# Kernel optimization log

Measured on AMD Instinct MI355X. Metric: run time of the kernel, lower is better.

The kernel has to match this reference:

```python
import jax, jax.numpy as jnp
import numpy as np

INPUT_DIM = 80
ENC_DIM = 256
ATTN_DIM = 128
GRU_DIM = 256
B = 32
T_ENC = 800
T_DEC = 400


def setup_inputs() -> dict:
    key = jax.random.key(0)
    ks = jax.random.split(key, 12)
    s = 0.05
    d = {}
    d['enc_feat'] = jax.random.normal(ks[0], (B, T_ENC, ENC_DIM), jnp.float32)
    d['ground_truth'] = jax.random.normal(ks[1], (B, T_DEC, INPUT_DIM), jnp.float32)
    # GRU (PyTorch layout): weight_ih (3*G, in), weight_hh (3*G, G)
    d['W_ih'] = jax.random.normal(ks[2], (3 * GRU_DIM, INPUT_DIM + ENC_DIM), jnp.float32) * s
    d['W_hh'] = jax.random.normal(ks[3], (3 * GRU_DIM, GRU_DIM), jnp.float32) * s
    d['b_ih'] = jax.random.normal(ks[4], (3 * GRU_DIM,), jnp.float32) * s
    d['b_hh'] = jax.random.normal(ks[5], (3 * GRU_DIM,), jnp.float32) * s
    # Additive attention: v^T tanh(W_enc e + W_dec h + b)
    d['W_enc'] = jax.random.normal(ks[6], (ATTN_DIM, ENC_DIM), jnp.float32) * s
    d['W_dec'] = jax.random.normal(ks[7], (ATTN_DIM, GRU_DIM), jnp.float32) * s
    d['b_attn'] = jax.random.normal(ks[8], (ATTN_DIM,), jnp.float32) * s
    d['v_attn'] = jax.random.normal(ks[9], (ATTN_DIM,), jnp.float32) * s
    # output_trans: Linear(gru_dim + enc_feat_dim -> input_dim)
    d['W_out'] = jax.random.normal(ks[10], (INPUT_DIM, GRU_DIM + ENC_DIM), jnp.float32) * s
    d['b_out'] = jax.random.normal(ks[11], (INPUT_DIM,), jnp.float32) * s
    return d


def reference(enc_feat, ground_truth, W_ih, W_hh, b_ih, b_hh,
              W_enc, W_dec, b_attn, v_attn, W_out, b_out):
    # Teacher-forced decode (teacher_force_rate=1.0): max_step = T_dec,
    # input at each step is ground_truth[:, t, :].
    Bsz, T_enc, E = enc_feat.shape
    G = W_hh.shape[1]
    # Encoder projection for additive attention (step-invariant)
    enc_proj = jnp.einsum('bte,ae->bta', enc_feat, W_enc)  # (B, T_enc, attn_dim)

    def step(carry, x_t):
        h, ctx = carry  # h: (B,G), ctx: (B,E)
        inp = jnp.concatenate([x_t, ctx], axis=-1)  # (B, input_dim+E)
        gi = inp @ W_ih.T + b_ih
        gh = h @ W_hh.T + b_hh
        ir, iz, inn = jnp.split(gi, 3, axis=-1)
        hr, hz, hn = jnp.split(gh, 3, axis=-1)
        r = jax.nn.sigmoid(ir + hr)
        z = jax.nn.sigmoid(iz + hz)
        n = jnp.tanh(inn + r * hn)
        h_new = (1.0 - z) * n + z * h  # PyTorch GRU update
        # additive attention over encoder timesteps
        dec_proj = h_new @ W_dec.T + b_attn  # (B, attn_dim)
        scores = jnp.einsum('bta,a->bt', jnp.tanh(enc_proj + dec_proj[:, None, :]), v_attn)
        attn = jax.nn.softmax(scores, axis=-1)  # (B, T_enc)
        ctx_new = jnp.einsum('bt,bte->be', attn, enc_feat)  # (B, E)
        concat = jnp.concatenate([h_new, ctx_new], axis=-1)
        pred = jax.nn.log_softmax(concat @ W_out.T + b_out, axis=-1)
        return (h_new, ctx_new), (pred, attn)

    h0 = jnp.zeros((Bsz, G), enc_feat.dtype)
    c0 = jnp.zeros((Bsz, E), enc_feat.dtype)
    xs = jnp.swapaxes(ground_truth, 0, 1)  # (T_dec, B, input_dim)
    _, (preds, attns) = jax.lax.scan(step, (h0, c0), xs)
    pred_seq = jnp.swapaxes(preds, 0, 1)    # (B, T_dec, input_dim)
    attn_record = jnp.swapaxes(attns, 0, 1)  # (B, T_dec, T_enc)
    return pred_seq, attn_record
```

## Files before the change

### kernel.cpp

```cpp
#include <hip/hip_runtime.h>

#define BB    32
#define TDEC  400
#define TENC  800
#define EDIM  256
#define GDIM  256
#define ADIM  128
#define IDIM  80
#define G3    768
#define NSL   16
#define SLH   16
#define SLT   50
#define FSTR  16
#define EPST  136
#define ETST  58

typedef unsigned short u16;
typedef unsigned int u32;

__device__ __forceinline__ float b2f(u16 u) {
  union { u32 i; float f; } x; x.i = ((u32)u) << 16; return x.f;
}
__device__ __forceinline__ u16 f2b(float f) {
  union { float f; u32 u; } x; x.f = f;
  u32 u = x.u; u += 0x7fffu + ((u >> 16) & 1u);
  return (u16)(u >> 16);
}
__device__ __forceinline__ void ld8(const u16* p, float* w) {
  const uint4 q = *reinterpret_cast<const uint4*>(p);
  union { u32 i; float f; } c;
  c.i = q.x << 16;          w[0] = c.f;
  c.i = q.x & 0xffff0000u;  w[1] = c.f;
  c.i = q.y << 16;          w[2] = c.f;
  c.i = q.y & 0xffff0000u;  w[3] = c.f;
  c.i = q.z << 16;          w[4] = c.f;
  c.i = q.z & 0xffff0000u;  w[5] = c.f;
  c.i = q.w << 16;          w[6] = c.f;
  c.i = q.w & 0xffff0000u;  w[7] = c.f;
}
__device__ __forceinline__ void ldf8(const float* p, float* w) {
  const float4 a = *reinterpret_cast<const float4*>(p);
  const float4 b = *reinterpret_cast<const float4*>(p + 4);
  w[0] = a.x; w[1] = a.y; w[2] = a.z; w[3] = a.w;
  w[4] = b.x; w[5] = b.y; w[6] = b.z; w[7] = b.w;
}
__device__ __forceinline__ float fsigmoid(float x) {
  return __builtin_amdgcn_rcpf(1.f + __expf(-x));
}
__device__ __forceinline__ float ftanh(float x) {
  float e = __expf(2.f * x);
  return 1.f - 2.f * __builtin_amdgcn_rcpf(e + 1.f);
}
__device__ __forceinline__ void ast(float* p, float v) {
  __hip_atomic_store(p, v, __ATOMIC_RELAXED, __HIP_MEMORY_SCOPE_AGENT);
}
__device__ __forceinline__ float ald(const float* p) {
  return __hip_atomic_load(p, __ATOMIC_RELAXED, __HIP_MEMORY_SCOPE_AGENT);
}
__device__ __forceinline__ void aadd(float* p, float v) {
  (void)__hip_atomic_fetch_add(p, v, __ATOMIC_RELAXED, __HIP_MEMORY_SCOPE_AGENT);
}

__global__ __launch_bounds__(256) void k_gix(
    const float* __restrict__ gt, const float* __restrict__ W_ih,
    const float* __restrict__ b_ih, u16* __restrict__ gi_x) {
  __shared__ float sc_x[8][IDIM];
  const int tid = threadIdx.x;
  const int b = blockIdx.x / 50;
  const int t0 = (blockIdx.x % 50) * 8;
  for (int idx = tid; idx < 8 * IDIM; idx += 256) {
    int row = idx / IDIM, col = idx % IDIM;
    sc_x[row][col] = gt[((size_t)b * TDEC + t0 + row) * IDIM + col];
  }
  __syncthreads();
  for (int kk = 0; kk < 3; ++kk) {
    const int g = tid + 256 * kk;
    const float* wrow = W_ih + (size_t)g * 336;
    float acc[8] = {0,0,0,0,0,0,0,0};
    #pragma unroll 2
    for (int k8 = 0; k8 < IDIM / 8; ++k8) {
      float w[8]; ldf8(wrow + (k8 << 3), w);
      #pragma unroll
      for (int tt = 0; tt < 8; ++tt) {
        const float* x = &sc_x[tt][k8 << 3];
        acc[tt] += w[0]*x[0] + w[1]*x[1] + w[2]*x[2] + w[3]*x[3]
                 + w[4]*x[4] + w[5]*x[5] + w[6]*x[6] + w[7]*x[7];
      }
    }
    const float bias = b_ih[g];
    #pragma unroll
    for (int tt = 0; tt < 8; ++tt)
      gi_x[((size_t)b * TDEC + t0 + tt) * G3 + g] = f2b(acc[tt] + bias);
  }
}

__global__ __launch_bounds__(256) void k_encp(
    const float* __restrict__ enc_feat, const float* __restrict__ W_enc,
    u16* __restrict__ encp, u16* __restrict__ enc_bf) {
  __shared__ float sc_x[16][EDIM];
  const int tid = threadIdx.x;
  const int b = blockIdx.x / 50;
  const int te0 = (blockIdx.x % 50) * 16;
  for (int idx = tid; idx < 16 * EDIM; idx += 256) {
    int row = idx >> 8, col = idx & 255;
    sc_x[row][col] = enc_feat[((size_t)b * TENC + te0 + row) * EDIM + col];
  }
  __syncthreads();
  const int a = tid & 127;
  const int tg = tid >> 7;
  const float* wrow = W_enc + (size_t)a * EDIM;
  float acc[8] = {0,0,0,0,0,0,0,0};
  #pragma unroll 4
  for (int k8 = 0; k8 < EDIM / 8; ++k8) {
    float w[8]; ldf8(wrow + (k8 << 3), w);
    #pragma unroll
    for (int tt = 0; tt < 8; ++tt) {
      const float* x = &sc_x[tg * 8 + tt][k8 << 3];
      acc[tt] += w[0]*x[0] + w[1]*x[1] + w[2]*x[2] + w[3]*x[3]
               + w[4]*x[4] + w[5]*x[5] + w[6]*x[6] + w[7]*x[7];
    }
  }
  #pragma unroll
  for (int tt = 0; tt < 8; ++tt)
    encp[((size_t)b * TENC + te0 + tg * 8 + tt) * ADIM + a] = f2b(acc[tt]);
  for (int idx = tid; idx < 16 * EDIM; idx += 256)
    enc_bf[((size_t)b * TENC + te0) * EDIM + idx] = f2b(sc_x[idx >> 8][idx & 255]);
}

__global__ __launch_bounds__(256, 2) void k_decode(
    const float* __restrict__ W_ih, const float* __restrict__ W_hh,
    const float* __restrict__ b_hh, const float* __restrict__ W_dec,
    const float* __restrict__ b_attn, const float* __restrict__ v_attn,
    const u16* __restrict__ gi_x, const u16* __restrict__ encp,
    const u16* __restrict__ enc_bf, float* __restrict__ stash,
    float* __restrict__ Xh, float* __restrict__ Dacc,
    float* __restrict__ Xctxacc, float* __restrict__ Xsumacc,
    int* __restrict__ flagA, int* __restrict__ flagB,
    float* __restrict__ out_attn) {
  __shared__ __align__(16) u16 encp_lds[SLT * EPST];
  __shared__ __align__(16) u16 enc_t[EDIM * ETST];
  __shared__ u32 sWdp[128 * 9];
  __shared__ __align__(16) float sc_h[256];
  __shared__ float sc_ing[4][68];
  __shared__ float sc_inh[4][68];
  __shared__ float sc_dec[ADIM];
  __shared__ float sc_g0[48];
  __shared__ float sc_g1[48];
  __shared__ float sc_w[56];
  __shared__ float sc_v[ADIM];
  __shared__ float sc_ba[ADIM];
  __shared__ float sc_bhh[48];
  __shared__ float sc_gx[48];
  __shared__ float sc_xs[4];

  const int tid = threadIdx.x;
  const int b = blockIdx.x & 31;
  const int j = blockIdx.x >> 5;
  const int lane = tid & 63;
  const int bank = j & 3;

  u32 wctx[32], whh[32];
  #pragma unroll
  for (int i = 0; i < 32; ++i) { wctx[i] = 0u; whh[i] = 0u; }
  if (tid < 192) {
    const int r = tid >> 2, q = tid & 3;
    const int grow = (r >> 4) * 256 + SLH * j + (r & 15);
    const float2* s1 = reinterpret_cast<const float2*>(
        W_ih + (size_t)grow * 336 + 80 + q * 64);
    const float2* s2 = reinterpret_cast<const float2*>(
        W_hh + (size_t)grow * 256 + q * 64);
    #pragma unroll
    for (int i = 0; i < 32; ++i) {
      const float2 v1 = s1[i], v2 = s2[i];
      wctx[i] = (u32)f2b(v1.x) | ((u32)f2b(v1.y) << 16);
      whh[i]  = (u32)f2b(v2.x) | ((u32)f2b(v2.y) << 16);
    }
  }
  for (int idx = tid; idx < 128 * 8; idx += 256) {
    const int a = idx >> 3, k2 = idx & 7;
    const float2 v = *reinterpret_cast<const float2*>(
        W_dec + (size_t)a * GDIM + SLH * j + 2 * k2);
    sWdp[a * 9 + k2] = (u32)f2b(v.x) | ((u32)f2b(v.y) << 16);
  }
  for (int idx = tid; idx < SLT * ADIM; idx += 256) {
    const int te = idx >> 7, a = idx & 127;
    encp_lds[te * EPST + a] = encp[((size_t)b * TENC + SLT * j + te) * ADIM + a];
  }
  for (int idx = tid; idx < SLT * EDIM; idx += 256) {
    const int te = idx >> 8, e = idx & 255;
    enc_t[e * ETST + te] = enc_bf[((size_t)b * TENC + SLT * j + te) * EDIM + e];
  }
  if (tid < ADIM) { sc_v[tid] = v_attn[tid]; sc_ba[tid] = b_attn[tid]; }
  if (tid < 48) {
    const int gate = tid >> 4, i = tid & 15;
    const int grow = gate * 256 + SLH * j + i;
    const float bh = b_hh[grow];
    sc_bhh[tid] = bh;
    sc_g1[tid] = bh;
    sc_gx[tid] = b2f(gi_x[((size_t)b * TDEC + 0) * G3 + grow]);
  }
  sc_h[tid] = 0.f;
  sc_ing[tid >> 6][tid & 63] = 0.f;
  sc_inh[tid >> 6][tid & 63] = 0.f;
  __syncthreads();

  for (int t = 0; t < TDEC; ++t) {
    const int p = t & 1;
    if (tid < 192) {
      const float* act = &sc_ing[tid & 3][0];
      float acc = 0.f;
      #pragma unroll
      for (int i = 0; i < 32; ++i) {
        union { u32 u; float f; } lo, hi;
        lo.u = wctx[i] << 16; hi.u = wctx[i] & 0xffff0000u;
        acc += lo.f * act[2 * i] + hi.f * act[2 * i + 1];
      }
      acc += __shfl_xor(acc, 1);
      acc += __shfl_xor(acc, 2);
      if ((tid & 3) == 0) sc_g0[tid >> 2] = acc + sc_gx[tid >> 2];
    }
    __syncthreads();
    if (tid < 64) {
      float hval = 0.f;
      if (lane < SLH) {
        const float gr = sc_g0[lane] + sc_g1[lane];
        const float gz = sc_g0[SLH + lane] + sc_g1[SLH + lane];
        const float rr = fsigmoid(gr);
        const float zz = fsigmoid(gz);
        const float nn = ftanh(sc_g0[2 * SLH + lane] + rr * sc_g1[2 * SLH + lane]);
        const float hp = sc_h[SLH * j + lane];
        hval = (1.f - zz) * nn + zz * hp;
        ast(&Xh[b * GDIM + SLH * j + lane], hval);
      }
      float hn16[16];
      #pragma unroll
      for (int k = 0; k < 16; ++k) hn16[k] = __shfl(hval, k);
      #pragma unroll
      for (int r2 = 0; r2 < 2; ++r2) {
        const int a = lane + 64 * r2;
        const u32* wp = &sWdp[a * 9];
        float acc = 0.f;
        #pragma unroll
        for (int k2 = 0; k2 < 8; ++k2) {
          const u32 w2 = wp[k2];
          union { u32 u; float f; } lo, hi;
          lo.u = w2 << 16; hi.u = w2 & 0xffff0000u;
          acc += lo.f * hn16[2 * k2] + hi.f * hn16[2 * k2 + 1];
        }
        aadd(&Dacc[((p * BB + b) * 4 + bank) * ADIM + a], acc);
      }
    }
    __syncthreads();
    if (tid == 0)
      __hip_atomic_store(&flagA[(b * NSL + j) * FSTR], t + 1, __ATOMIC_RELAXED,
                         __HIP_MEMORY_SCOPE_AGENT);
    if (tid < NSL) {
      const int* fp = &flagA[(b * NSL + tid) * FSTR];
      while (__hip_atomic_load(fp, __ATOMIC_RELAXED,
                               __HIP_MEMORY_SCOPE_AGENT) < t + 1)
        __builtin_amdgcn_s_sleep(1);
    }
    __syncthreads();
    {
      const float hv = ald(&Xh[b * GDIM + tid]);
      sc_h[tid] = hv;
      sc_inh[tid >> 6][tid & 63] = hv;
      if (j == 0) stash[((size_t)b * TDEC + t) * 512 + tid] = hv;
    }
    if (tid < ADIM) {
      float d = sc_ba[tid];
      #pragma unroll
      for (int k = 0; k < 4; ++k)
        d += ald(&Dacc[((p * BB + b) * 4 + k) * ADIM + tid]);
      sc_dec[tid] = d;
    }
    if (tid < 64) {
      const int w = j * 64 + tid;
      ast(&Xctxacc[(((1 - p) * BB + b) * 4 + (w >> 8)) * EDIM + (w & 255)], 0.f);
    } else if (tid < 96) {
      const int w = j * 32 + (tid - 64);
      ast(&Dacc[(((1 - p) * BB + b) * 4 + (w >> 7)) * ADIM + (w & 127)], 0.f);
    } else if (tid == 96 && j < 4) {
      ast(&Xsumacc[(((1 - p) * BB + b) * 4 + j) * FSTR], 0.f);
    }
    __syncthreads();
    if (tid < 200) {
      const int te = tid >> 2, q4 = tid & 3;
      const u16* ep = &encp_lds[te * EPST + q4 * 32];
      const float* dp = sc_dec + q4 * 32;
      const float* vp = sc_v + q4 * 32;
      float s = 0.f;
      #pragma unroll
      for (int k8 = 0; k8 < 4; ++k8) {
        float w[8]; ld8(ep + (k8 << 3), w);
        #pragma unroll
        for (int i = 0; i < 8; ++i) {
          const int a = (k8 << 3) + i;
          s += ftanh(w[i] + dp[a]) * vp[a];
        }
      }
      s += __shfl_xor(s, 1);
      s += __shfl_xor(s, 2);
      if (q4 == 0) sc_w[te] = __expf(s);
    } else if (tid < 248) {
      const int gl = tid - 200;
      const int grow = (gl >> 4) * 256 + SLH * j + (gl & 15);
      const int tn = (t + 1 < TDEC) ? t + 1 : t;
      sc_gx[gl] = b2f(gi_x[((size_t)b * TDEC + tn) * G3 + grow]);
    }
    __syncthreads();
    if (tid < 64) {
      float v = (tid < SLT) ? sc_w[tid] : 0.f;
      #pragma unroll
      for (int off = 1; off < 64; off <<= 1) v += __shfl_xor(v, off);
      if (tid == 0) aadd(&Xsumacc[((p * BB + b) * 4 + bank) * FSTR], v);
    }
    {
      const u32* et = reinterpret_cast<const u32*>(&enc_t[tid * ETST]);
      float pc = 0.f;
      #pragma unroll
      for (int k2 = 0; k2 < 25; ++k2) {
        const u32 w2 = et[k2];
        union { u32 u; float f; } lo, hi;
        lo.u = w2 << 16; hi.u = w2 & 0xffff0000u;
        pc += sc_w[2 * k2] * lo.f + sc_w[2 * k2 + 1] * hi.f;
      }
      aadd(&Xctxacc[((p * BB + b) * 4 + bank) * EDIM + tid], pc);
    }
    if (tid < 192) {
      const float* act = &sc_inh[tid & 3][0];
      float acc = 0.f;
      #pragma unroll
      for (int i = 0; i < 32; ++i) {
        union { u32 u; float f; } lo, hi;
        lo.u = whh[i] << 16; hi.u = whh[i] & 0xffff0000u;
        acc += lo.f * act[2 * i] + hi.f * act[2 * i + 1];
      }
      acc += __shfl_xor(acc, 1);
      acc += __shfl_xor(acc, 2);
      if ((tid & 3) == 0) sc_g1[tid >> 2] = acc + sc_bhh[tid >> 2];
    }
    __syncthreads();
    if (tid == 0)
      __hip_atomic_store(&flagB[(b * NSL + j) * FSTR], t + 1, __ATOMIC_RELAXED,
                         __HIP_MEMORY_SCOPE_AGENT);
    if (tid < NSL) {
      const int* fp = &flagB[(b * NSL + tid) * FSTR];
      while (__hip_atomic_load(fp, __ATOMIC_RELAXED,
                               __HIP_MEMORY_SCOPE_AGENT) < t + 1)
        __builtin_amdgcn_s_sleep(1);
      if (tid < 4) sc_xs[tid] = ald(&Xsumacc[((p * BB + b) * 4 + tid) * FSTR]);
    }
    __syncthreads();
    {
      const float S = sc_xs[0] + sc_xs[1] + sc_xs[2] + sc_xs[3];
      float c = 0.f;
      #pragma unroll
      for (int k = 0; k < 4; ++k)
        c += ald(&Xctxacc[((p * BB + b) * 4 + k) * EDIM + tid]);
      const float invS = __builtin_amdgcn_rcpf(S);
      const float cv = c * invS;
      sc_ing[tid >> 6][tid & 63] = cv;
      if (j == 0) stash[((size_t)b * TDEC + t) * 512 + 256 + tid] = cv;
      if (tid < SLT)
        out_attn[((size_t)b * TDEC + t) * TENC + SLT * j + tid] =
            sc_w[tid] * invS;
    }
    __syncthreads();
  }
}

__global__ __launch_bounds__(256) void k_pred(
    const float* __restrict__ stash, const float* __restrict__ W_out,
    const float* __restrict__ b_out, float* __restrict__ out_pred) {
  __shared__ float sc_s[4][512];
  __shared__ float sc_lp[2][4][IDIM];
  __shared__ float sc_l[4][IDIM];
  __shared__ float sc_lse[4];
  const int tid = threadIdx.x;
  const int b = blockIdx.x / 100;
  const int t0 = (blockIdx.x % 100) * 4;
  for (int idx = tid; idx < 4 * 512; idx += 256)
    sc_s[idx >> 9][idx & 511] = stash[((size_t)b * TDEC + t0) * 512 + idx];
  __syncthreads();
  const int o = tid & 127, kh = tid >> 7;
  if (o < IDIM) {
    const float* wrow = W_out + (size_t)o * 512 + kh * 256;
    float acc[4] = {0,0,0,0};
    #pragma unroll 4
    for (int k8 = 0; k8 < 32; ++k8) {
      float w[8]; ldf8(wrow + (k8 << 3), w);
      #pragma unroll
      for (int tt = 0; tt < 4; ++tt) {
        const float* x = &sc_s[tt][kh * 256 + (k8 << 3)];
        acc[tt] += w[0]*x[0] + w[1]*x[1] + w[2]*x[2] + w[3]*x[3]
                 + w[4]*x[4] + w[5]*x[5] + w[6]*x[6] + w[7]*x[7];
      }
    }
    #pragma unroll
    for (int tt = 0; tt < 4; ++tt) sc_lp[kh][tt][o] = acc[tt];
  }
  __syncthreads();
  if (tid < IDIM) {
    const float bb = b_out[tid];
    #pragma unroll
    for (int tt = 0; tt < 4; ++tt)
      sc_l[tt][tid] = sc_lp[0][tt][tid] + sc_lp[1][tt][tid] + bb;
  }
  __syncthreads();
  {
    const int w = tid >> 6, lane = tid & 63;
    const float a0 = sc_l[w][lane];
    const float a1 = (lane < IDIM - 64) ? sc_l[w][lane + 64] : -1e30f;
    float m = fmaxf(a0, a1);
    #pragma unroll
    for (int off = 1; off < 64; off <<= 1) m = fmaxf(m, __shfl_xor(m, off));
    float e = __expf(a0 - m) + ((lane < IDIM - 64) ? __expf(a1 - m) : 0.f);
    #pragma unroll
    for (int off = 1; off < 64; off <<= 1) e += __shfl_xor(e, off);
    if (lane == 0) sc_lse[w] = m + __logf(e);
  }
  __syncthreads();
  for (int idx = tid; idx < 4 * IDIM; idx += 256) {
    const int tt = idx / IDIM, oo = idx % IDIM;
    out_pred[((size_t)b * TDEC + t0 + tt) * IDIM + oo] =
        sc_l[tt][oo] - sc_lse[tt];
  }
}

extern "C" void kernel_launch(void* const* d_in, const int* in_sizes, int n_in,
                              void* d_out, int out_size, void* d_ws, size_t ws_size,
                              hipStream_t stream) {
  const float* enc_feat = (const float*)d_in[0];
  const float* gt       = (const float*)d_in[1];
  const float* W_ih     = (const float*)d_in[2];
  const float* W_hh     = (const float*)d_in[3];
  const float* b_ih     = (const float*)d_in[4];
  const float* b_hh     = (const float*)d_in[5];
  const float* W_enc    = (const float*)d_in[6];
  const float* W_dec    = (const float*)d_in[7];
  const float* b_attn   = (const float*)d_in[8];
  const float* v_attn   = (const float*)d_in[9];
  const float* W_out    = (const float*)d_in[10];
  const float* b_out    = (const float*)d_in[11];
  float* out_pred = (float*)d_out;
  float* out_attn = out_pred + (size_t)BB * TDEC * IDIM;

  char* ws = (char*)d_ws;
  size_t off = 0;
  u16* gi_x   = (u16*)(ws + off);   off += (size_t)BB * TDEC * G3 * 2;
  u16* encp   = (u16*)(ws + off);   off += (size_t)BB * TENC * ADIM * 2;
  u16* enc_bf = (u16*)(ws + off);   off += (size_t)BB * TENC * EDIM * 2;
  float* stash= (float*)(ws + off); off += (size_t)BB * TDEC * 512 * 4;
  float* Xh   = (float*)(ws + off); off += (size_t)BB * GDIM * 4;
  char* zbase = ws + off;
  int* flagA    = (int*)(ws + off);   off += (size_t)BB * NSL * FSTR * 4;
  int* flagB    = (int*)(ws + off);   off += (size_t)BB * NSL * FSTR * 4;
  float* Dacc   = (float*)(ws + off); off += (size_t)BB * 2 * 4 * ADIM * 4;
  float* Xctxacc= (float*)(ws + off); off += (size_t)BB * 2 * 4 * EDIM * 4;
  float* Xsumacc= (float*)(ws + off); off += (size_t)BB * 2 * 4 * FSTR * 4;
  const size_t zbytes = (size_t)(ws + off - zbase);

  hipMemsetAsync(zbase, 0, zbytes, stream);

  hipLaunchKernelGGL(k_gix, dim3(BB * 50), dim3(256), 0, stream,
                     gt, W_ih, b_ih, gi_x);
  hipLaunchKernelGGL(k_encp, dim3(BB * 50), dim3(256), 0, stream,
                     enc_feat, W_enc, encp, enc_bf);
  hipLaunchKernelGGL(k_decode, dim3(BB * NSL), dim3(256), 0, stream,
                     W_ih, W_hh, b_hh, W_dec, b_attn, v_attn,
                     gi_x, encp, enc_bf, stash, Xh, Dacc, Xctxacc, Xsumacc,
                     flagA, flagB, out_attn);
  hipLaunchKernelGGL(k_pred, dim3(BB * 100), dim3(256), 0, stream,
                     stash, W_out, b_out, out_pred);
}
```

Before: 3.388 ms.

## Halve decode slices per batch using 512-thread blocks with dynamic LDS

The persistent decode kernel now splits each batch row into 8 slices instead of 16. Each block runs 512 threads and owns 32 hidden units and 100 encoder timesteps. Encoder tiles move to dynamic shared memory, and per-slice arrays, the W_dec tile and thread-role ranges are resized to match. The aim is to cut the number of blocks taking part in each per-step cross-block flag barrier and the atomic partial-sum traffic. The cost is more per-block work and larger LDS use, and all 256 blocks must still be co-resident.

```diff
diff --git a/kernel.cpp b/kernel.cpp
--- a/kernel.cpp
+++ b/kernel.cpp
@@ -8,12 +8,12 @@
 #define ADIM  128
 #define IDIM  80
 #define G3    768
-#define NSL   16
-#define SLH   16
-#define SLT   50
+#define NSL   8
+#define SLH   32
+#define SLT   100
 #define FSTR  16
 #define EPST  136
-#define ETST  58
+#define ETST  102
 
 typedef unsigned short u16;
 typedef unsigned int u32;
@@ -127,7 +127,7 @@
     enc_bf[((size_t)b * TENC + te0) * EDIM + idx] = f2b(sc_x[idx >> 8][idx & 255]);
 }
 
-__global__ __launch_bounds__(256, 2) void k_decode(
+__global__ __launch_bounds__(512, 1) void k_decode(
     const float* __restrict__ W_ih, const float* __restrict__ W_hh,
     const float* __restrict__ b_hh, const float* __restrict__ W_dec,
     const float* __restrict__ b_attn, const float* __restrict__ v_attn,
@@ -137,20 +137,22 @@
     float* __restrict__ Xctxacc, float* __restrict__ Xsumacc,
     int* __restrict__ flagA, int* __restrict__ flagB,
     float* __restrict__ out_attn) {
-  __shared__ __align__(16) u16 encp_lds[SLT * EPST];
-  __shared__ __align__(16) u16 enc_t[EDIM * ETST];
-  __shared__ u32 sWdp[128 * 9];
+  extern __shared__ __align__(16) u16 dynlds[];
+  u16* encp_lds = dynlds;
+  u16* enc_t    = dynlds + SLT * EPST;
+
+  __shared__ u32 sWdp[ADIM * 17];
   __shared__ __align__(16) float sc_h[256];
   __shared__ float sc_ing[4][68];
   __shared__ float sc_inh[4][68];
   __shared__ float sc_dec[ADIM];
-  __shared__ float sc_g0[48];
-  __shared__ float sc_g1[48];
-  __shared__ float sc_w[56];
+  __shared__ float sc_g0[96];
+  __shared__ float sc_g1[96];
+  __shared__ float sc_w[104];
   __shared__ float sc_v[ADIM];
   __shared__ float sc_ba[ADIM];
-  __shared__ float sc_bhh[48];
-  __shared__ float sc_gx[48];
+  __shared__ float sc_bhh[96];
+  __shared__ float sc_gx[96];
   __shared__ float sc_xs[4];
 
   const int tid = threadIdx.x;
@@ -162,9 +164,9 @@
   u32 wctx[32], whh[32];
   #pragma unroll
   for (int i = 0; i < 32; ++i) { wctx[i] = 0u; whh[i] = 0u; }
-  if (tid < 192) {
+  if (tid < 384) {
     const int r = tid >> 2, q = tid & 3;
-    const int grow = (r >> 4) * 256 + SLH * j + (r & 15);
+    const int grow = (r >> 5) * 256 + SLH * j + (r & 31);
     const float2* s1 = reinterpret_cast<const float2*>(
         W_ih + (size_t)grow * 336 + 80 + q * 64);
     const float2* s2 = reinterpret_cast<const float2*>(
@@ -176,37 +178,38 @@
       whh[i]  = (u32)f2b(v2.x) | ((u32)f2b(v2.y) << 16);
     }
   }
-  for (int idx = tid; idx < 128 * 8; idx += 256) {
-    const int a = idx >> 3, k2 = idx & 7;
+  for (int idx = tid; idx < ADIM * 16; idx += 512) {
+    const int a = idx >> 4, k2 = idx & 15;
     const float2 v = *reinterpret_cast<const float2*>(
         W_dec + (size_t)a * GDIM + SLH * j + 2 * k2);
-    sWdp[a * 9 + k2] = (u32)f2b(v.x) | ((u32)f2b(v.y) << 16);
-  }
-  for (int idx = tid; idx < SLT * ADIM; idx += 256) {
+    sWdp[a * 17 + k2] = (u32)f2b(v.x) | ((u32)f2b(v.y) << 16);
+  }
+  for (int idx = tid; idx < SLT * ADIM; idx += 512) {
     const int te = idx >> 7, a = idx & 127;
     encp_lds[te * EPST + a] = encp[((size_t)b * TENC + SLT * j + te) * ADIM + a];
   }
-  for (int idx = tid; idx < SLT * EDIM; idx += 256) {
+  for (int idx = tid; idx < SLT * EDIM; idx += 512) {
     const int te = idx >> 8, e = idx & 255;
     enc_t[e * ETST + te] = enc_bf[((size_t)b * TENC + SLT * j + te) * EDIM + e];
   }
   if (tid < ADIM) { sc_v[tid] = v_attn[tid]; sc_ba[tid] = b_attn[tid]; }
-  if (tid < 48) {
-    const int gate = tid >> 4, i = tid & 15;
-    const int grow = gate * 256 + SLH * j + i;
+  if (tid < 96) {
+    const int grow = (tid >> 5) * 256 + SLH * j + (tid & 31);
     const float bh = b_hh[grow];
     sc_bhh[tid] = bh;
     sc_g1[tid] = bh;
     sc_gx[tid] = b2f(gi_x[((size_t)b * TDEC + 0) * G3 + grow]);
   }
-  sc_h[tid] = 0.f;
-  sc_ing[tid >> 6][tid & 63] = 0.f;
-  sc_inh[tid >> 6][tid & 63] = 0.f;
+  if (tid < 256) {
+    sc_h[tid] = 0.f;
+    sc_ing[tid >> 6][tid & 63] = 0.f;
+    sc_inh[tid >> 6][tid & 63] = 0.f;
+  }
   __syncthreads();
 
   for (int t = 0; t < TDEC; ++t) {
     const int p = t & 1;
-    if (tid < 192) {
+    if (tid < 384) {
       const float* act = &sc_ing[tid & 3][0];
       float acc = 0.f;
       #pragma unroll
@@ -232,20 +235,20 @@
         hval = (1.f - zz) * nn + zz * hp;
         ast(&Xh[b * GDIM + SLH * j + lane], hval);
       }
-      float hn16[16];
-      #pragma unroll
-      for (int k = 0; k < 16; ++k) hn16[k] = __shfl(hval, k);
+      float hn[32];
+      #pragma unroll
+      for (int k = 0; k < 32; ++k) hn[k] = __shfl(hval, k);
       #pragma unroll
       for (int r2 = 0; r2 < 2; ++r2) {
         const int a = lane + 64 * r2;
-        const u32* wp = &sWdp[a * 9];
+        const u32* wp = &sWdp[a * 17];
         float acc = 0.f;
         #pragma unroll
-        for (int k2 = 0; k2 < 8; ++k2) {
+        for (int k2 = 0; k2 < 16; ++k2) {
           const u32 w2 = wp[k2];
           union { u32 u; float f; } lo, hi;
           lo.u = w2 << 16; hi.u = w2 & 0xffff0000u;
-          acc += lo.f * hn16[2 * k2] + hi.f * hn16[2 * k2 + 1];
+          acc += lo.f * hn[2 * k2] + hi.f * hn[2 * k2 + 1];
         }
         aadd(&Dacc[((p * BB + b) * 4 + bank) * ADIM + a], acc);
       }
@@ -261,7 +264,7 @@
         __builtin_amdgcn_s_sleep(1);
     }
     __syncthreads();
-    {
+    if (tid < 256) {
       const float hv = ald(&Xh[b * GDIM + tid]);
       sc_h[tid] = hv;
       sc_inh[tid >> 6][tid & 63] = hv;
@@ -274,17 +277,17 @@
         d += ald(&Dacc[((p * BB + b) * 4 + k) * ADIM + tid]);
       sc_dec[tid] = d;
     }
-    if (tid < 64) {
-      const int w = j * 64 + tid;
+    if (tid >= 256 && tid < 384) {
+      const int w = j * 128 + (tid - 256);
       ast(&Xctxacc[(((1 - p) * BB + b) * 4 + (w >> 8)) * EDIM + (w & 255)], 0.f);
-    } else if (tid < 96) {
-      const int w = j * 32 + (tid - 64);
+    } else if (tid >= 384 && tid < 448) {
+      const int w = j * 64 + (tid - 384);
       ast(&Dacc[(((1 - p) * BB + b) * 4 + (w >> 7)) * ADIM + (w & 127)], 0.f);
-    } else if (tid == 96 && j < 4) {
+    } else if (tid == 448 && j < 4) {
       ast(&Xsumacc[(((1 - p) * BB + b) * 4 + j) * FSTR], 0.f);
     }
     __syncthreads();
-    if (tid < 200) {
+    if (tid < 400) {
       const int te = tid >> 2, q4 = tid & 3;
       const u16* ep = &encp_lds[te * EPST + q4 * 32];
       const float* dp = sc_dec + q4 * 32;
@@ -302,24 +305,31 @@
       s += __shfl_xor(s, 1);
       s += __shfl_xor(s, 2);
       if (q4 == 0) sc_w[te] = __expf(s);
-    } else if (tid < 248) {
-      const int gl = tid - 200;
-      const int grow = (gl >> 4) * 256 + SLH * j + (gl & 15);
+    } else if (tid >= 448) {
       const int tn = (t + 1 < TDEC) ? t + 1 : t;
-      sc_gx[gl] = b2f(gi_x[((size_t)b * TDEC + tn) * G3 + grow]);
+      const int gl = tid - 448;
+      {
+        const int grow = (gl >> 5) * 256 + SLH * j + (gl & 31);
+        sc_gx[gl] = b2f(gi_x[((size_t)b * TDEC + tn) * G3 + grow]);
+      }
+      if (gl < 32) {
+        const int g2 = gl + 64;
+        const int grow = (g2 >> 5) * 256 + SLH * j + (g2 & 31);
+        sc_gx[g2] = b2f(gi_x[((size_t)b * TDEC + tn) * G3 + grow]);
+      }
     }
     __syncthreads();
     if (tid < 64) {
-      float v = (tid < SLT) ? sc_w[tid] : 0.f;
+      float v = (lane < 50) ? sc_w[lane] + sc_w[lane + 50] : 0.f;
       #pragma unroll
       for (int off = 1; off < 64; off <<= 1) v += __shfl_xor(v, off);
-      if (tid == 0) aadd(&Xsumacc[((p * BB + b) * 4 + bank) * FSTR], v);
-    }
-    {
+      if (lane == 0) aadd(&Xsumacc[((p * BB + b) * 4 + bank) * FSTR], v);
+    }
+    if (tid < 256) {
       const u32* et = reinterpret_cast<const u32*>(&enc_t[tid * ETST]);
       float pc = 0.f;
       #pragma unroll
-      for (int k2 = 0; k2 < 25; ++k2) {
+      for (int k2 = 0; k2 < 50; ++k2) {
         const u32 w2 = et[k2];
         union { u32 u; float f; } lo, hi;
         lo.u = w2 << 16; hi.u = w2 & 0xffff0000u;
@@ -327,7 +337,7 @@
       }
       aadd(&Xctxacc[((p * BB + b) * 4 + bank) * EDIM + tid], pc);
     }
-    if (tid < 192) {
+    if (tid < 384) {
       const float* act = &sc_inh[tid & 3][0];
       float acc = 0.f;
       #pragma unroll
@@ -354,14 +364,16 @@
     __syncthreads();
     {
       const float S = sc_xs[0] + sc_xs[1] + sc_xs[2] + sc_xs[3];
-      float c = 0.f;
-      #pragma unroll
-      for (int k = 0; k < 4; ++k)
-        c += ald(&Xctxacc[((p * BB + b) * 4 + k) * EDIM + tid]);
       const float invS = __builtin_amdgcn_rcpf(S);
-      const float cv = c * invS;
-      sc_ing[tid >> 6][tid & 63] = cv;
-      if (j == 0) stash[((size_t)b * TDEC + t) * 512 + 256 + tid] = cv;
+      if (tid < 256) {
+        float c = 0.f;
+        #pragma unroll
+        for (int k = 0; k < 4; ++k)
+          c += ald(&Xctxacc[((p * BB + b) * 4 + k) * EDIM + tid]);
+        const float cv = c * invS;
+        sc_ing[tid >> 6][tid & 63] = cv;
+        if (j == 0) stash[((size_t)b * TDEC + t) * 512 + 256 + tid] = cv;
+      }
       if (tid < SLT)
         out_attn[((size_t)b * TDEC + t) * TENC + SLT * j + tid] =
             sc_w[tid] * invS;
@@ -461,13 +473,21 @@
   float* Xsumacc= (float*)(ws + off); off += (size_t)BB * 2 * 4 * FSTR * 4;
   const size_t zbytes = (size_t)(ws + off - zbase);
 
+  const int DYNB = (SLT * EPST + EDIM * ETST) * 2;
+  static bool s_attr = false;
+  if (!s_attr) {
+    (void)hipFuncSetAttribute(reinterpret_cast<const void*>(k_decode),
+                              hipFuncAttributeMaxDynamicSharedMemorySize, DYNB);
+    s_attr = true;
+  }
+
   hipMemsetAsync(zbase, 0, zbytes, stream);
 
   hipLaunchKernelGGL(k_gix, dim3(BB * 50), dim3(256), 0, stream,
                      gt, W_ih, b_ih, gi_x);
   hipLaunchKernelGGL(k_encp, dim3(BB * 50), dim3(256), 0, stream,
                      enc_feat, W_enc, encp, enc_bf);
-  hipLaunchKernelGGL(k_decode, dim3(BB * NSL), dim3(256), 0, stream,
+  hipLaunchKernelGGL(k_decode, dim3(BB * NSL), dim3(512), DYNB, stream,
                      W_ih, W_hh, b_hh, W_dec, b_attn, v_attn,
                      gi_x, encp, enc_bf, stash, Xh, Dacc, Xctxacc, Xsumacc,
                      flagA, flagB, out_attn);
```

New measurement: 3.239 ms. 4.4% less time.
